# Kernel tuning notes

Hardware: AMD Instinct MI355X
Metric: run time of the kernel (lower is better)

Reference implementation:

```python
import jax, jax.numpy as jnp
import numpy as np

B, S, I, H = 64, 512, 1024, 1024
MOG_ITERS = 4


def setup_inputs() -> dict:
    key = jax.random.key(0)
    ks = jax.random.split(key, 8)
    sI = 1.0 / np.sqrt(I)
    sH = 1.0 / np.sqrt(H)
    return {
        "x": jax.random.normal(ks[0], (B, S, I), dtype=jnp.float32),
        "h0": jnp.zeros((B, H), dtype=jnp.float32),
        "c0": jnp.zeros((B, H), dtype=jnp.float32),
        "Wih": jax.random.normal(ks[1], (I, 4 * H), dtype=jnp.float32) * sI,
        "Whh": jax.random.normal(ks[2], (H, 4 * H), dtype=jnp.float32) * sH,
        "bih": jnp.zeros((4 * H,), dtype=jnp.float32),
        "bhh": jnp.zeros((4 * H,), dtype=jnp.float32),
        "Q": jax.random.normal(ks[3], (H, I), dtype=jnp.float32) * sH,
        "R": jax.random.normal(ks[4], (I, H), dtype=jnp.float32) * sI,
    }


def _mogrify(xt, ht, Q, R):
    # alternating mogrifier rounds: odd i updates xt, even i updates ht
    for i in range(1, MOG_ITERS + 1):
        if i % 2 == 0:
            ht = 2.0 * jax.nn.sigmoid(xt @ R) * ht
        else:
            xt = 2.0 * jax.nn.sigmoid(ht @ Q) * xt
    return xt, ht


def reference(x, h0, c0, Wih, Whh, bih, bhh, Q, R):
    def step(carry, xt):
        ht, Ct = carry
        xt, ht = _mogrify(xt, ht, Q, R)
        gates = xt @ Wih + bih + ht @ Whh + bhh  # [B, 4H]
        i_g, f_g, g_g, o_g = jnp.split(gates, 4, axis=-1)
        Ct = jax.nn.sigmoid(f_g) * Ct + jax.nn.sigmoid(i_g) * jnp.tanh(g_g)
        ht = jax.nn.sigmoid(o_g) * jnp.tanh(Ct)
        return (ht, Ct), ht

    xs = jnp.swapaxes(x, 0, 1)  # [S, B, I]
    (ht, Ct), hs = jax.lax.scan(step, (h0, c0), xs)
    hidden_seq = jnp.swapaxes(hs, 0, 1)  # [B, S, H]
    return hidden_seq, (ht, Ct)
```

## Files before the change

kernel.cpp:

```cpp
#include <hip/hip_runtime.h>
#include <stdint.h>

#define B_ 64
#define S_ 512
#define I_ 1024
#define H_ 1024

typedef __attribute__((ext_vector_type(8))) short bf16x8;
typedef __attribute__((ext_vector_type(4))) float f32x4;

#define BAR_OFF   0u
#define BIAS_OFF  4096u
#define XT_OFF    32768u
#define HT0_OFF   (XT_OFF + 262144u)
#define HT1_OFF   (HT0_OFF + 262144u)
#define QT_OFF    (1u << 20)
#define RT_OFF    (5u << 20)
#define GT_OFF    (9u << 20)
#define APLANE    65536
#define QPLANE    (1024 * 1024)
#define GPLANE    (4096 * 2048)
#define GGATE     (1024 * 2048)

__device__ inline float bf2f(uint16_t u) {
    uint32_t v = ((uint32_t)u) << 16; float f; __builtin_memcpy(&f, &v, 4); return f;
}
__device__ inline uint16_t f2bf(float f) {
    uint32_t v; __builtin_memcpy(&v, &f, 4);
    v = (v + 0x7FFFu + ((v >> 16) & 1u)) >> 16;
    return (uint16_t)v;
}
__device__ inline void f2hilo(float v, uint16_t& hi, uint16_t& lo) {
    hi = f2bf(v);
    lo = f2bf(v - bf2f(hi));
}
__device__ inline float sigmf(float x) { return 1.0f / (1.0f + __expf(-x)); }

__device__ inline bf16x8 cload16(const uint16_t* p) {
    union { unsigned long long q[2]; bf16x8 v; } u;
    u.q[0] = __hip_atomic_load((const unsigned long long*)p,
                               __ATOMIC_RELAXED, __HIP_MEMORY_SCOPE_AGENT);
    u.q[1] = __hip_atomic_load((const unsigned long long*)p + 1,
                               __ATOMIC_RELAXED, __HIP_MEMORY_SCOPE_AGENT);
    return u.v;
}
__device__ inline void cstore2(uint16_t* p, uint16_t v) {
    asm volatile("global_store_short %0, %1, off sc0 sc1"
                 :: "v"(p), "v"((uint32_t)v) : "memory");
}

__global__ __launch_bounds__(256)
void transpose_f32(const float* __restrict__ src, uint16_t* __restrict__ dstHi,
                   uint16_t* __restrict__ dstLo, int N, int dstStride, int dstColOff)
{
    __shared__ float tile[64][65];
    int k0 = blockIdx.x * 64;
    int n0 = blockIdx.y * 64;
    for (int i = threadIdx.x; i < 4096; i += 256) {
        int rr = i >> 6, cc = i & 63;
        tile[rr][cc] = src[(int64_t)(k0 + rr) * N + n0 + cc];
    }
    __syncthreads();
    for (int i = threadIdx.x; i < 4096; i += 256) {
        int rr = i >> 6, cc = i & 63;
        float v = tile[cc][rr];
        uint16_t hi, lo; f2hilo(v, hi, lo);
        int64_t o = (int64_t)(n0 + rr) * dstStride + dstColOff + k0 + cc;
        dstHi[o] = hi; dstLo[o] = lo;
    }
}

__global__ __launch_bounds__(256)
void bias_kernel(const float* __restrict__ a, const float* __restrict__ b,
                 float* __restrict__ o)
{
    int i = blockIdx.x * 256 + threadIdx.x;
    if (i < 4096) o[i] = a[i] + b[i];
}

__global__ __launch_bounds__(256, 1)
void mog_lstm(const float* __restrict__ x,
              const float* __restrict__ h0,
              const float* __restrict__ c0,
              const uint16_t* __restrict__ Qt,
              const uint16_t* __restrict__ Rt,
              const uint16_t* __restrict__ Gt,
              const float*    __restrict__ biasf,
              uint16_t* __restrict__ xtb,
              uint16_t* __restrict__ ht0b,
              uint16_t* __restrict__ ht1b,
              uint32_t* __restrict__ bar,
              float* __restrict__ out)
{
    const int tid  = threadIdx.x;
    const int lane = tid & 63;
    const int wave = tid >> 6;
    const int blk  = blockIdx.x;
    const int r    = (blk >> 3) & 3;
    const int c    = (blk & 7) * 8 + (blk >> 5);
    const int q4   = lane >> 4;
    const int cl   = lane & 15;
    const int kOff = q4 * 8;

    __shared__ float part[4][4][16][16];
    __shared__ float Ct_s[16][16];
    __shared__ float xsh[16][16];
    __shared__ float hsh[16][16];

    uint32_t* cnt = bar + r * 64;
    uint32_t bt = 0;
    uint32_t dead = 0;

    auto gbar = [&]() {
        bt += 64;
        __syncthreads();
        if (tid == 0) {
            asm volatile("s_waitcnt vmcnt(0)" ::: "memory");
            __hip_atomic_fetch_add(cnt, 1u, __ATOMIC_RELAXED, __HIP_MEMORY_SCOPE_AGENT);
            if (!dead) {
                const uint64_t tw = __builtin_amdgcn_s_memrealtime();
                while (__hip_atomic_load(cnt, __ATOMIC_RELAXED, __HIP_MEMORY_SCOPE_AGENT) < bt) {
                    __builtin_amdgcn_s_sleep(2);
                    if (__builtin_amdgcn_s_memrealtime() - tw > 40000000ull) {
                        dead = 1; break;
                    }
                }
            }
            asm volatile("" ::: "memory");
        }
        __syncthreads();
    };

    auto mogp = [&](const uint16_t* __restrict__ Ahi, const uint16_t* __restrict__ Whi,
                    const float* gF, int64_t gFs, uint16_t* gHi, float (*sh)[16]) {
        const int64_t aoff = (int64_t)(r * 16 + cl) * 1024 + wave * 256 + kOff;
        const int64_t boff = (int64_t)(c * 16 + cl) * 1024 + wave * 256 + kOff;
        const uint16_t* ah = Ahi + aoff;
        const uint16_t* al = Ahi + APLANE + aoff;
        const uint16_t* bh = Whi + boff;
        const uint16_t* bl = Whi + QPLANE + boff;
        f32x4 acc = {0.f, 0.f, 0.f, 0.f};
#pragma unroll
        for (int k = 0; k < 256; k += 32) {
            bf16x8 vah = cload16(ah + k);
            bf16x8 val = cload16(al + k);
            bf16x8 vbh = *(const bf16x8*)(bh + k);
            bf16x8 vbl = *(const bf16x8*)(bl + k);
            acc = __builtin_amdgcn_mfma_f32_16x16x32_bf16(vah, vbh, acc, 0, 0, 0);
            acc = __builtin_amdgcn_mfma_f32_16x16x32_bf16(vah, vbl, acc, 0, 0, 0);
            acc = __builtin_amdgcn_mfma_f32_16x16x32_bf16(val, vbh, acc, 0, 0, 0);
        }
#pragma unroll
        for (int i = 0; i < 4; ++i) part[wave][0][q4 * 4 + i][cl] = acc[i];
        __syncthreads();
        if (wave == 0) {
#pragma unroll
            for (int i = 0; i < 4; ++i) {
                int row = q4 * 4 + i;
                float u = part[0][0][row][cl] + part[1][0][row][cl]
                        + part[2][0][row][cl] + part[3][0][row][cl];
                float gm = 2.0f * sigmf(u);
                float oldv = gF ? __builtin_nontemporal_load(gF + (int64_t)row * gFs + cl)
                                : sh[row][cl];
                float nv = gm * oldv;
                sh[row][cl] = nv;
                uint16_t hi, lo; f2hilo(nv, hi, lo);
                cstore2(gHi + row * 1024 + cl, hi);
                cstore2(gHi + APLANE + row * 1024 + cl, lo);
            }
        }
    };

    if (wave == 0) {
#pragma unroll
        for (int i = 0; i < 4; ++i) {
            int row = q4 * 4 + i;
            int grow = r * 16 + row, gcol = c * 16 + cl;
            float hv = h0[grow * 1024 + gcol];
            uint16_t hi, lo; f2hilo(hv, hi, lo);
            cstore2(ht0b + grow * 1024 + gcol, hi);
            cstore2(ht0b + APLANE + grow * 1024 + gcol, lo);
            hsh[row][cl] = hv;
            Ct_s[row][cl] = c0[grow * 1024 + gcol];
        }
    }
    gbar();

    for (int t = 0; t < S_; ++t) {
        const int p = t & 1;
        uint16_t* htp = p ? ht1b : ht0b;
        uint16_t* htn = p ? ht0b : ht1b;
        uint16_t* xsl = xtb + (r * 16) * 1024 + c * 16;
        uint16_t* hsl = htp + (r * 16) * 1024 + c * 16;
        const float* xsrc = x + (int64_t)(r * 16) * (S_ * I_) + (int64_t)t * I_ + c * 16;

        mogp(htp, Qt, xsrc, (int64_t)S_ * I_, xsl, xsh); gbar();
        mogp(xtb, Rt, nullptr, 0, hsl, hsh);             gbar();
        mogp(htp, Qt, nullptr, 0, xsl, xsh);             gbar();
        mogp(xtb, Rt, nullptr, 0, hsl, hsh);             gbar();

        {
            const int64_t arow = (int64_t)(r * 16 + cl) * 1024 + wave * 256 + kOff;
            const uint16_t* axh = xtb + arow;
            const uint16_t* axl = xtb + APLANE + arow;
            const uint16_t* ahh = htp + arow;
            const uint16_t* ahl = htp + APLANE + arow;
            const uint16_t* gB = Gt + (int64_t)(c * 16 + cl) * 2048 + wave * 256 + kOff;
            f32x4 accg[4] = {{0.f,0.f,0.f,0.f},{0.f,0.f,0.f,0.f},
                             {0.f,0.f,0.f,0.f},{0.f,0.f,0.f,0.f}};
#pragma unroll 4
            for (int k = 0; k < 256; k += 32) {
                bf16x8 vxh = cload16(axh + k);
                bf16x8 vxl = cload16(axl + k);
                bf16x8 vhh = cload16(ahh + k);
                bf16x8 vhl = cload16(ahl + k);
#pragma unroll
                for (int g = 0; g < 4; ++g) {
                    const uint16_t* bx = gB + (int64_t)g * GGATE + k;
                    bf16x8 bxh = *(const bf16x8*)(bx);
                    bf16x8 bxl = *(const bf16x8*)(bx + GPLANE);
                    f32x4 a = accg[g];
                    a = __builtin_amdgcn_mfma_f32_16x16x32_bf16(vxh, bxh, a, 0, 0, 0);
                    a = __builtin_amdgcn_mfma_f32_16x16x32_bf16(vxh, bxl, a, 0, 0, 0);
                    a = __builtin_amdgcn_mfma_f32_16x16x32_bf16(vxl, bxh, a, 0, 0, 0);
                    bf16x8 bhh2 = *(const bf16x8*)(bx + 1024);
                    bf16x8 bhl2 = *(const bf16x8*)(bx + GPLANE + 1024);
                    a = __builtin_amdgcn_mfma_f32_16x16x32_bf16(vhh, bhh2, a, 0, 0, 0);
                    a = __builtin_amdgcn_mfma_f32_16x16x32_bf16(vhh, bhl2, a, 0, 0, 0);
                    a = __builtin_amdgcn_mfma_f32_16x16x32_bf16(vhl, bhh2, a, 0, 0, 0);
                    accg[g] = a;
                }
            }
#pragma unroll
            for (int g = 0; g < 4; ++g)
#pragma unroll
                for (int i = 0; i < 4; ++i)
                    part[wave][g][q4 * 4 + i][cl] = accg[g][i];
            __syncthreads();
            if (wave == 0) {
                const int gcol = c * 16 + cl;
                const float bi = biasf[gcol];
                const float bf = biasf[1024 + gcol];
                const float bg = biasf[2048 + gcol];
                const float bo = biasf[3072 + gcol];
#pragma unroll
                for (int i = 0; i < 4; ++i) {
                    int row = q4 * 4 + i;
                    float gi = part[0][0][row][cl] + part[1][0][row][cl]
                             + part[2][0][row][cl] + part[3][0][row][cl] + bi;
                    float gf = part[0][1][row][cl] + part[1][1][row][cl]
                             + part[2][1][row][cl] + part[3][1][row][cl] + bf;
                    float gg = part[0][2][row][cl] + part[1][2][row][cl]
                             + part[2][2][row][cl] + part[3][2][row][cl] + bg;
                    float go = part[0][3][row][cl] + part[1][3][row][cl]
                             + part[2][3][row][cl] + part[3][3][row][cl] + bo;
                    float ii = sigmf(gi), ff = sigmf(gf);
                    float g2 = tanhf(gg), oo = sigmf(go);
                    float Cn = ff * Ct_s[row][cl] + ii * g2;
                    float hh = oo * tanhf(Cn);
                    Ct_s[row][cl] = Cn;
                    hsh[row][cl] = hh;
                    int grow = r * 16 + row;
                    uint16_t hi, lo; f2hilo(hh, hi, lo);
                    cstore2(htn + grow * 1024 + gcol, hi);
                    cstore2(htn + APLANE + grow * 1024 + gcol, lo);
                    __builtin_nontemporal_store(hh,
                        out + (int64_t)grow * (S_ * H_) + (int64_t)t * H_ + gcol);
                    if (t == S_ - 1)
                        out[(int64_t)B_ * S_ * H_ + grow * H_ + gcol] = hh;
                }
            }
        }
        gbar();
    }

    if (wave == 0) {
#pragma unroll
        for (int i = 0; i < 4; ++i) {
            int row = q4 * 4 + i;
            int grow = r * 16 + row, gcol = c * 16 + cl;
            out[(int64_t)B_ * S_ * H_ + (int64_t)B_ * H_ + grow * H_ + gcol] = Ct_s[row][cl];
        }
    }
}

extern "C" void kernel_launch(void* const* d_in, const int* in_sizes, int n_in,
                              void* d_out, int out_size, void* d_ws, size_t ws_size,
                              hipStream_t stream)
{
    (void)in_sizes; (void)n_in; (void)out_size; (void)ws_size;
    const float* x   = (const float*)d_in[0];
    const float* h0  = (const float*)d_in[1];
    const float* c0  = (const float*)d_in[2];
    const float* Wih = (const float*)d_in[3];
    const float* Whh = (const float*)d_in[4];
    const float* bih = (const float*)d_in[5];
    const float* bhh = (const float*)d_in[6];
    const float* Q   = (const float*)d_in[7];
    const float* R   = (const float*)d_in[8];

    char* ws = (char*)d_ws;
    uint32_t* bar   = (uint32_t*)(ws + BAR_OFF);
    float*    biasf = (float*)(ws + BIAS_OFF);
    uint16_t* xtb   = (uint16_t*)(ws + XT_OFF);
    uint16_t* ht0b  = (uint16_t*)(ws + HT0_OFF);
    uint16_t* ht1b  = (uint16_t*)(ws + HT1_OFF);
    uint16_t* Qt    = (uint16_t*)(ws + QT_OFF);
    uint16_t* Rt    = (uint16_t*)(ws + RT_OFF);
    uint16_t* Gt    = (uint16_t*)(ws + GT_OFF);

    (void)hipMemsetAsync(ws + BAR_OFF, 0, 4096, stream);
    bias_kernel<<<16, 256, 0, stream>>>(bih, bhh, biasf);
    transpose_f32<<<dim3(16, 16), 256, 0, stream>>>(Q,   Qt, Qt + QPLANE, 1024, 1024, 0);
    transpose_f32<<<dim3(16, 16), 256, 0, stream>>>(R,   Rt, Rt + QPLANE, 1024, 1024, 0);
    transpose_f32<<<dim3(16, 64), 256, 0, stream>>>(Wih, Gt, Gt + GPLANE, 4096, 2048, 0);
    transpose_f32<<<dim3(16, 64), 256, 0, stream>>>(Whh, Gt, Gt + GPLANE, 4096, 2048, 1024);
    mog_lstm<<<256, 256, 0, stream>>>(x, h0, c0, Qt, Rt, Gt, biasf,
                                      xtb, ht0b, ht1b, bar, (float*)d_out);
}
```

Before: 30.60 ms.

## Spread epilogue across all waves, batch coherent A loads, drop barrier waitcnt

The per-phase epilogue (sigmoid gating, LSTM cell update, hi/lo stores) now runs on all four waves, one element per lane, instead of wave 0 looping over four rows while the other waves idle. Activation operands are loaded up front into register arrays with 8-byte coherent loads before the MFMA loop, so their latency overlaps instead of being serialized per k-step. Bias loads are hoisted out of the time loop. The explicit vmcnt(0) wait before the barrier atomic is removed, which risks other blocks seeing stale stores, and the larger register arrays may raise register pressure.

```diff
diff --git a/kernel.cpp b/kernel.cpp
--- a/kernel.cpp
+++ b/kernel.cpp
@@ -8,6 +8,7 @@
 
 typedef __attribute__((ext_vector_type(8))) short bf16x8;
 typedef __attribute__((ext_vector_type(4))) float f32x4;
+typedef unsigned long long u64;
 
 #define BAR_OFF   0u
 #define BIAS_OFF  4096u
@@ -36,18 +37,15 @@
 }
 __device__ inline float sigmf(float x) { return 1.0f / (1.0f + __expf(-x)); }
 
-__device__ inline bf16x8 cload16(const uint16_t* p) {
-    union { unsigned long long q[2]; bf16x8 v; } u;
-    u.q[0] = __hip_atomic_load((const unsigned long long*)p,
-                               __ATOMIC_RELAXED, __HIP_MEMORY_SCOPE_AGENT);
-    u.q[1] = __hip_atomic_load((const unsigned long long*)p + 1,
-                               __ATOMIC_RELAXED, __HIP_MEMORY_SCOPE_AGENT);
-    return u.v;
+__device__ inline u64 cload8(const uint16_t* p) {
+    return __hip_atomic_load((const u64*)p, __ATOMIC_RELAXED, __HIP_MEMORY_SCOPE_AGENT);
 }
 __device__ inline void cstore2(uint16_t* p, uint16_t v) {
     asm volatile("global_store_short %0, %1, off sc0 sc1"
                  :: "v"(p), "v"((uint32_t)v) : "memory");
 }
+
+union U2 { u64 q[2]; bf16x8 v; };
 
 __global__ __launch_bounds__(256)
 void transpose_f32(const float* __restrict__ src, uint16_t* __restrict__ dstHi,
@@ -101,6 +99,8 @@
     const int q4   = lane >> 4;
     const int cl   = lane & 15;
     const int kOff = q4 * 8;
+    const int erow = wave * 4 + q4;
+    const int ecol = cl;
 
     __shared__ float part[4][4][16][16];
     __shared__ float Ct_s[16][16];
@@ -115,7 +115,6 @@
         bt += 64;
         __syncthreads();
         if (tid == 0) {
-            asm volatile("s_waitcnt vmcnt(0)" ::: "memory");
             __hip_atomic_fetch_add(cnt, 1u, __ATOMIC_RELAXED, __HIP_MEMORY_SCOPE_AGENT);
             if (!dead) {
                 const uint64_t tw = __builtin_amdgcn_s_memrealtime();
@@ -131,60 +130,74 @@
         __syncthreads();
     };
 
-    auto mogp = [&](const uint16_t* __restrict__ Ahi, const uint16_t* __restrict__ Whi,
-                    const float* gF, int64_t gFs, uint16_t* gHi, float (*sh)[16]) {
+    auto aload = [&](u64* av, const uint16_t* Abase) {
         const int64_t aoff = (int64_t)(r * 16 + cl) * 1024 + wave * 256 + kOff;
-        const int64_t boff = (int64_t)(c * 16 + cl) * 1024 + wave * 256 + kOff;
-        const uint16_t* ah = Ahi + aoff;
-        const uint16_t* al = Ahi + APLANE + aoff;
-        const uint16_t* bh = Whi + boff;
-        const uint16_t* bl = Whi + QPLANE + boff;
-        f32x4 acc = {0.f, 0.f, 0.f, 0.f};
-#pragma unroll
-        for (int k = 0; k < 256; k += 32) {
-            bf16x8 vah = cload16(ah + k);
-            bf16x8 val = cload16(al + k);
-            bf16x8 vbh = *(const bf16x8*)(bh + k);
-            bf16x8 vbl = *(const bf16x8*)(bl + k);
-            acc = __builtin_amdgcn_mfma_f32_16x16x32_bf16(vah, vbh, acc, 0, 0, 0);
-            acc = __builtin_amdgcn_mfma_f32_16x16x32_bf16(vah, vbl, acc, 0, 0, 0);
-            acc = __builtin_amdgcn_mfma_f32_16x16x32_bf16(val, vbh, acc, 0, 0, 0);
-        }
-#pragma unroll
-        for (int i = 0; i < 4; ++i) part[wave][0][q4 * 4 + i][cl] = acc[i];
+#pragma unroll
+        for (int k8 = 0; k8 < 8; ++k8) {
+            const uint16_t* ph = Abase + aoff + k8 * 32;
+            const uint16_t* pl = Abase + APLANE + aoff + k8 * 32;
+            av[4 * k8 + 0] = cload8(ph);
+            av[4 * k8 + 1] = cload8(ph + 4);
+            av[4 * k8 + 2] = cload8(pl);
+            av[4 * k8 + 3] = cload8(pl + 4);
+        }
+    };
+
+    auto mogp = [&](const uint16_t* Abase, const uint16_t* Whi,
+                    const float* gF, int64_t gFs, uint16_t* gSlice,
+                    float (*sh)[16]) {
+        u64 av[32];
+        aload(av, Abase);
+        {
+            const int64_t boff = (int64_t)(c * 16 + cl) * 1024 + wave * 256 + kOff;
+            const uint16_t* bh = Whi + boff;
+            const uint16_t* bl = Whi + QPLANE + boff;
+            f32x4 acc = {0.f, 0.f, 0.f, 0.f};
+#pragma unroll
+            for (int k8 = 0; k8 < 8; ++k8) {
+                U2 uh, ul;
+                uh.q[0] = av[4 * k8 + 0]; uh.q[1] = av[4 * k8 + 1];
+                ul.q[0] = av[4 * k8 + 2]; ul.q[1] = av[4 * k8 + 3];
+                bf16x8 vbh = *(const bf16x8*)(bh + k8 * 32);
+                bf16x8 vbl = *(const bf16x8*)(bl + k8 * 32);
+                acc = __builtin_amdgcn_mfma_f32_16x16x32_bf16(uh.v, vbh, acc, 0, 0, 0);
+                acc = __builtin_amdgcn_mfma_f32_16x16x32_bf16(uh.v, vbl, acc, 0, 0, 0);
+                acc = __builtin_amdgcn_mfma_f32_16x16x32_bf16(ul.v, vbh, acc, 0, 0, 0);
+            }
+#pragma unroll
+            for (int i = 0; i < 4; ++i) part[wave][0][q4 * 4 + i][cl] = acc[i];
+        }
         __syncthreads();
-        if (wave == 0) {
-#pragma unroll
-            for (int i = 0; i < 4; ++i) {
-                int row = q4 * 4 + i;
-                float u = part[0][0][row][cl] + part[1][0][row][cl]
-                        + part[2][0][row][cl] + part[3][0][row][cl];
-                float gm = 2.0f * sigmf(u);
-                float oldv = gF ? __builtin_nontemporal_load(gF + (int64_t)row * gFs + cl)
-                                : sh[row][cl];
-                float nv = gm * oldv;
-                sh[row][cl] = nv;
-                uint16_t hi, lo; f2hilo(nv, hi, lo);
-                cstore2(gHi + row * 1024 + cl, hi);
-                cstore2(gHi + APLANE + row * 1024 + cl, lo);
-            }
+        {
+            float u = part[0][0][erow][ecol] + part[1][0][erow][ecol]
+                    + part[2][0][erow][ecol] + part[3][0][erow][ecol];
+            float gm = 2.0f * sigmf(u);
+            float oldv = gF ? __builtin_nontemporal_load(gF + (int64_t)erow * gFs + ecol)
+                            : sh[erow][ecol];
+            float nv = gm * oldv;
+            sh[erow][ecol] = nv;
+            uint16_t hi, lo; f2hilo(nv, hi, lo);
+            cstore2(gSlice + erow * 1024 + ecol, hi);
+            cstore2(gSlice + APLANE + erow * 1024 + ecol, lo);
         }
     };
 
-    if (wave == 0) {
-#pragma unroll
-        for (int i = 0; i < 4; ++i) {
-            int row = q4 * 4 + i;
-            int grow = r * 16 + row, gcol = c * 16 + cl;
-            float hv = h0[grow * 1024 + gcol];
-            uint16_t hi, lo; f2hilo(hv, hi, lo);
-            cstore2(ht0b + grow * 1024 + gcol, hi);
-            cstore2(ht0b + APLANE + grow * 1024 + gcol, lo);
-            hsh[row][cl] = hv;
-            Ct_s[row][cl] = c0[grow * 1024 + gcol];
-        }
+    {
+        int grow = r * 16 + erow, gcol = c * 16 + ecol;
+        float hv = h0[grow * 1024 + gcol];
+        uint16_t hi, lo; f2hilo(hv, hi, lo);
+        cstore2(ht0b + grow * 1024 + gcol, hi);
+        cstore2(ht0b + APLANE + grow * 1024 + gcol, lo);
+        hsh[erow][ecol] = hv;
+        Ct_s[erow][ecol] = c0[grow * 1024 + gcol];
     }
     gbar();
+
+    const int   gcol5 = c * 16 + ecol;
+    const float bi5 = biasf[gcol5];
+    const float bf5 = biasf[1024 + gcol5];
+    const float bg5 = biasf[2048 + gcol5];
+    const float bo5 = biasf[3072 + gcol5];
 
     for (int t = 0; t < S_; ++t) {
         const int p = t & 1;
@@ -200,34 +213,33 @@
         mogp(xtb, Rt, nullptr, 0, hsl, hsh);             gbar();
 
         {
-            const int64_t arow = (int64_t)(r * 16 + cl) * 1024 + wave * 256 + kOff;
-            const uint16_t* axh = xtb + arow;
-            const uint16_t* axl = xtb + APLANE + arow;
-            const uint16_t* ahh = htp + arow;
-            const uint16_t* ahl = htp + APLANE + arow;
+            u64 xa[32], ha[32];
+            aload(xa, xtb);
+            aload(ha, htp);
             const uint16_t* gB = Gt + (int64_t)(c * 16 + cl) * 2048 + wave * 256 + kOff;
             f32x4 accg[4] = {{0.f,0.f,0.f,0.f},{0.f,0.f,0.f,0.f},
                              {0.f,0.f,0.f,0.f},{0.f,0.f,0.f,0.f}};
-#pragma unroll 4
-            for (int k = 0; k < 256; k += 32) {
-                bf16x8 vxh = cload16(axh + k);
-                bf16x8 vxl = cload16(axl + k);
-                bf16x8 vhh = cload16(ahh + k);
-                bf16x8 vhl = cload16(ahl + k);
+#pragma unroll
+            for (int k8 = 0; k8 < 8; ++k8) {
+                U2 xh, xl, hh, hl;
+                xh.q[0] = xa[4 * k8 + 0]; xh.q[1] = xa[4 * k8 + 1];
+                xl.q[0] = xa[4 * k8 + 2]; xl.q[1] = xa[4 * k8 + 3];
+                hh.q[0] = ha[4 * k8 + 0]; hh.q[1] = ha[4 * k8 + 1];
+                hl.q[0] = ha[4 * k8 + 2]; hl.q[1] = ha[4 * k8 + 3];
 #pragma unroll
                 for (int g = 0; g < 4; ++g) {
-                    const uint16_t* bx = gB + (int64_t)g * GGATE + k;
+                    const uint16_t* bx = gB + (int64_t)g * GGATE + k8 * 32;
                     bf16x8 bxh = *(const bf16x8*)(bx);
                     bf16x8 bxl = *(const bf16x8*)(bx + GPLANE);
                     f32x4 a = accg[g];
-                    a = __builtin_amdgcn_mfma_f32_16x16x32_bf16(vxh, bxh, a, 0, 0, 0);
-                    a = __builtin_amdgcn_mfma_f32_16x16x32_bf16(vxh, bxl, a, 0, 0, 0);
-                    a = __builtin_amdgcn_mfma_f32_16x16x32_bf16(vxl, bxh, a, 0, 0, 0);
+                    a = __builtin_amdgcn_mfma_f32_16x16x32_bf16(xh.v, bxh, a, 0, 0, 0);
+                    a = __builtin_amdgcn_mfma_f32_16x16x32_bf16(xh.v, bxl, a, 0, 0, 0);
+                    a = __builtin_amdgcn_mfma_f32_16x16x32_bf16(xl.v, bxh, a, 0, 0, 0);
                     bf16x8 bhh2 = *(const bf16x8*)(bx + 1024);
                     bf16x8 bhl2 = *(const bf16x8*)(bx + GPLANE + 1024);
-                    a = __builtin_amdgcn_mfma_f32_16x16x32_bf16(vhh, bhh2, a, 0, 0, 0);
-                    a = __builtin_amdgcn_mfma_f32_16x16x32_bf16(vhh, bhl2, a, 0, 0, 0);
-                    a = __builtin_amdgcn_mfma_f32_16x16x32_bf16(vhl, bhh2, a, 0, 0, 0);
+                    a = __builtin_amdgcn_mfma_f32_16x16x32_bf16(hh.v, bhh2, a, 0, 0, 0);
+                    a = __builtin_amdgcn_mfma_f32_16x16x32_bf16(hh.v, bhl2, a, 0, 0, 0);
+                    a = __builtin_amdgcn_mfma_f32_16x16x32_bf16(hl.v, bhh2, a, 0, 0, 0);
                     accg[g] = a;
                 }
             }
@@ -236,51 +248,38 @@
 #pragma unroll
                 for (int i = 0; i < 4; ++i)
                     part[wave][g][q4 * 4 + i][cl] = accg[g][i];
-            __syncthreads();
-            if (wave == 0) {
-                const int gcol = c * 16 + cl;
-                const float bi = biasf[gcol];
-                const float bf = biasf[1024 + gcol];
-                const float bg = biasf[2048 + gcol];
-                const float bo = biasf[3072 + gcol];
-#pragma unroll
-                for (int i = 0; i < 4; ++i) {
-                    int row = q4 * 4 + i;
-                    float gi = part[0][0][row][cl] + part[1][0][row][cl]
-                             + part[2][0][row][cl] + part[3][0][row][cl] + bi;
-                    float gf = part[0][1][row][cl] + part[1][1][row][cl]
-                             + part[2][1][row][cl] + part[3][1][row][cl] + bf;
-                    float gg = part[0][2][row][cl] + part[1][2][row][cl]
-                             + part[2][2][row][cl] + part[3][2][row][cl] + bg;
-                    float go = part[0][3][row][cl] + part[1][3][row][cl]
-                             + part[2][3][row][cl] + part[3][3][row][cl] + bo;
-                    float ii = sigmf(gi), ff = sigmf(gf);
-                    float g2 = tanhf(gg), oo = sigmf(go);
-                    float Cn = ff * Ct_s[row][cl] + ii * g2;
-                    float hh = oo * tanhf(Cn);
-                    Ct_s[row][cl] = Cn;
-                    hsh[row][cl] = hh;
-                    int grow = r * 16 + row;
-                    uint16_t hi, lo; f2hilo(hh, hi, lo);
-                    cstore2(htn + grow * 1024 + gcol, hi);
-                    cstore2(htn + APLANE + grow * 1024 + gcol, lo);
-                    __builtin_nontemporal_store(hh,
-                        out + (int64_t)grow * (S_ * H_) + (int64_t)t * H_ + gcol);
-                    if (t == S_ - 1)
-                        out[(int64_t)B_ * S_ * H_ + grow * H_ + gcol] = hh;
-                }
-            }
+        }
+        __syncthreads();
+        {
+            float gi = part[0][0][erow][ecol] + part[1][0][erow][ecol]
+                     + part[2][0][erow][ecol] + part[3][0][erow][ecol] + bi5;
+            float gf = part[0][1][erow][ecol] + part[1][1][erow][ecol]
+                     + part[2][1][erow][ecol] + part[3][1][erow][ecol] + bf5;
+            float gg = part[0][2][erow][ecol] + part[1][2][erow][ecol]
+                     + part[2][2][erow][ecol] + part[3][2][erow][ecol] + bg5;
+            float go = part[0][3][erow][ecol] + part[1][3][erow][ecol]
+                     + part[2][3][erow][ecol] + part[3][3][erow][ecol] + bo5;
+            float ii = sigmf(gi), ff = sigmf(gf);
+            float g2 = tanhf(gg), oo = sigmf(go);
+            float Cn = ff * Ct_s[erow][ecol] + ii * g2;
+            float hh = oo * tanhf(Cn);
+            Ct_s[erow][ecol] = Cn;
+            hsh[erow][ecol] = hh;
+            int grow = r * 16 + erow;
+            uint16_t hi, lo; f2hilo(hh, hi, lo);
+            cstore2(htn + grow * 1024 + gcol5, hi);
+            cstore2(htn + APLANE + grow * 1024 + gcol5, lo);
+            __builtin_nontemporal_store(hh,
+                out + (int64_t)grow * (S_ * H_) + (int64_t)t * H_ + gcol5);
+            if (t == S_ - 1)
+                out[(int64_t)B_ * S_ * H_ + grow * H_ + gcol5] = hh;
         }
         gbar();
     }
 
-    if (wave == 0) {
-#pragma unroll
-        for (int i = 0; i < 4; ++i) {
-            int row = q4 * 4 + i;
-            int grow = r * 16 + row, gcol = c * 16 + cl;
-            out[(int64_t)B_ * S_ * H_ + (int64_t)B_ * H_ + grow * H_ + gcol] = Ct_s[row][cl];
-        }
+    {
+        int grow = r * 16 + erow;
+        out[(int64_t)B_ * S_ * H_ + (int64_t)B_ * H_ + grow * H_ + gcol5] = Ct_s[erow][ecol];
     }
 }
 
```

Result: faster. 28.09 ms (-8.2%).
